# Kernel optimization log

Hardware: AMD Instinct MI355X
Metric: run time of the kernel (lower is better)

Reference implementation:

```python
import jax, jax.numpy as jnp
import numpy as np

K_EDE = 10.0   # self.k
T_EDE = 0.1    # self.t
BN_EPS = 1e-5
T_A = 576.0    # 3*3*64, hardcoded in my_bn1/my_bn2


def qfn(x, prec):
    # dorefa-style round quantizer with straight-through gradient
    n = float(2 ** prec - 1)
    return x + jax.lax.stop_gradient(jnp.round(x * n) / n - x)


@jax.custom_vjp
def binary_quantize(x):
    return jnp.sign(x)


def _bq_fwd(x):
    return jnp.sign(x), x


def _bq_bwd(x, g):
    # IR-Net EDE backward: k * t * (1 - tanh(x*t)^2)
    return (K_EDE * T_EDE * (1.0 - jnp.tanh(x * T_EDE) ** 2) * g,)


binary_quantize.defvjp(_bq_fwd, _bq_bwd)


def _clip_T(x):
    T = jnp.maximum(jnp.abs(x.min()), jnp.abs(x.max()))
    return jax.lax.stop_gradient(jnp.clip(T, 1e-10, 255.0))


def quantize_conv_act(x, prec):
    # my_quantize_conv: clamp to [-T, T], scale to [-1,1], qfn (no rescale by T)
    T = _clip_T(x)
    return qfn(jnp.clip(x, -T, T) / T, prec)


def quantize(x, prec):
    # my_quantize: same but rescaled back by T
    T = _clip_T(x)
    return qfn(jnp.clip(x, -T, T) / T, prec) * T


def ir_conv2d(a, w, stride):
    # IR-Net 1w8a IRConv2d: per-out-channel normalize, binarize (sign), power-of-2 scale
    co = w.shape[0]
    wf = w.reshape(co, -1)
    bw = (w - wf.mean(1)[:, None, None, None]) / jnp.std(wf, axis=1, ddof=1)[:, None, None, None]
    sw = jax.lax.stop_gradient(
        2.0 ** jnp.round(jnp.log2(jnp.abs(bw.reshape(co, -1)).mean(1)))
    )[:, None, None, None]
    bw = binary_quantize(bw) * sw
    return jax.lax.conv_general_dilated(
        a, bw, window_strides=(stride, stride), padding=[(1, 1), (1, 1)],
        dimension_numbers=('NCHW', 'OIHW', 'NCHW'))


def bn_as_quantized_affine(x, gamma, beta, mean, var):
    # my_bn1/my_bn2 (eval mode): BN folded into per-channel scale+bias.
    # The original builds a CxC diagonal 1x1 conv; since off-diagonal entries are 0,
    # both the quantization stats (max|.|) and the conv reduce exactly to this
    # per-channel affine, which is the faithful fused form.
    std = jnp.sqrt(var + BN_EPS)
    w = gamma / std
    b = beta - w * mean
    qw = quantize(w, 3)
    qb = quantize(b, 12)
    aq = qfn(x / T_A, 10) * T_A  # my_quantize_activation(input, 10, T_a)
    return aq * qw[None, :, None, None] + qb[None, :, None, None]


def _block(x, w1, w2, g1, b1, m1, v1, g2, b2, m2, v2):
    xq = quantize_conv_act(x, 3)
    out = ir_conv2d(xq, w1, 1)
    out = bn_as_quantized_affine(out, g1, b1, m1, v1) + xq  # identity shortcut
    out = jnp.clip(out, -1.0, 1.0)  # hardtanh
    x1 = quantize_conv_act(out, 3)
    out = ir_conv2d(x1, w2, 1)
    out = bn_as_quantized_affine(out, g2, b2, m2, v2) + x1
    return jnp.clip(out, -1.0, 1.0)


def setup_inputs() -> dict:
    key = jax.random.key(0)
    ks = jax.random.split(key, 11)
    B, C, H, W = 128, 64, 56, 56
    return {
        'x': jax.random.normal(ks[0], (B, C, H, W), jnp.float32),
        'w1': jax.random.normal(ks[1], (C, C, 3, 3), jnp.float32) * 0.1,
        'w2': jax.random.normal(ks[2], (C, C, 3, 3), jnp.float32) * 0.1,
        'g1': jax.random.uniform(ks[3], (C,), jnp.float32, 0.5, 1.5),
        'b1': jax.random.normal(ks[4], (C,), jnp.float32) * 0.1,
        'm1': jax.random.normal(ks[5], (C,), jnp.float32) * 0.1,
        'v1': jax.random.uniform(ks[6], (C,), jnp.float32, 0.5, 1.5),
        'g2': jax.random.uniform(ks[7], (C,), jnp.float32, 0.5, 1.5),
        'b2': jax.random.normal(ks[8], (C,), jnp.float32) * 0.1,
        'm2': jax.random.normal(ks[9], (C,), jnp.float32) * 0.1,
        'v2': jax.random.uniform(ks[10], (C,), jnp.float32, 0.5, 1.5),
    }


def reference(x, w1, w2, g1, b1, m1, v1, g2, b2, m2, v2):
    return _block(x, w1, w2, g1, b1, m1, v1, g2, b2, m2, v2)
```

## Files before the change

### kernel.cpp

```cpp
#include <hip/hip_runtime.h>
#include <stdint.h>

typedef int v4i   __attribute__((ext_vector_type(4)));
typedef int v16i  __attribute__((ext_vector_type(16)));

#define B_    128
#define C_    64
#define H_    56
#define W_    56
#define HW_   3136
#define NELEM (B_*C_*HW_)

#define OFF_K0   0
#define OFF_K1   ((size_t)NELEM)
#define OFF_WB   ((size_t)2*NELEM)
#define OFF_PAR  (OFF_WB + 2*4*9*64*16)
#define OFF_MAX  (OFF_PAR + 384*4)

__device__ __forceinline__ float pw_reduce64(float r) {
    r = __fadd_rn(r, __shfl_xor(r, 1, 64));
    r = __fadd_rn(r, __shfl_xor(r, 2, 64));
    r = __fadd_rn(r, __shfl_xor(r, 4, 64));
    r = __fadd_rn(r, __shfl_xor(r, 8, 64));
    r = __fadd_rn(r, __shfl_xor(r, 16, 64));
    r = __fadd_rn(r, __shfl_xor(r, 32, 64));
    return r;
}

__global__ void k_pre(const float* __restrict__ x, unsigned* __restrict__ maxbits,
                      const float* __restrict__ w1, const float* __restrict__ w2,
                      int8_t* __restrict__ wb, float* __restrict__ par,
                      const float* __restrict__ g1, const float* __restrict__ bb1,
                      const float* __restrict__ mm1, const float* __restrict__ vv1,
                      const float* __restrict__ g2, const float* __restrict__ bb2,
                      const float* __restrict__ mm2, const float* __restrict__ vv2) {
    __shared__ float smax[4];
    const int b = blockIdx.x;
    const int tid = threadIdx.x;
    if (b < 1024) {
        float m = 0.f;
        const int n4 = NELEM / 4;
        for (int i = b * 256 + tid; i < n4; i += 1024 * 256) {
            float4 v = ((const float4*)x)[i];
            m = fmaxf(m, fmaxf(fmaxf(fabsf(v.x), fabsf(v.y)), fmaxf(fabsf(v.z), fabsf(v.w))));
        }
        for (int off = 32; off; off >>= 1) m = fmaxf(m, __shfl_down(m, off, 64));
        if ((tid & 63) == 0) smax[tid >> 6] = m;
        __syncthreads();
        if (tid == 0) {
            float mm = fmaxf(fmaxf(smax[0], smax[1]), fmaxf(smax[2], smax[3]));
            atomicMax(maxbits, __float_as_uint(mm));
        }
    } else if (b < 1056) {
        const int idx = (b - 1024) * 4 + (tid >> 6);
        const int layer = idx >> 6, co = idx & 63;
        const int lane = tid & 63;
        const float* w = (layer ? w2 : w1) + (size_t)co * 576;
        const int base = (lane >> 3) * 72 + (lane & 7);

        float v[9];
#pragma unroll
        for (int i = 0; i < 9; i++) v[i] = w[base + 8 * i];

        float s = v[0];
#pragma unroll
        for (int i = 1; i < 9; i++) s = __fadd_rn(s, v[i]);
        const float mean = __fdiv_rn(pw_reduce64(s), 576.0f);

        float d0 = __fsub_rn(v[0], mean);
        float sq = __fmul_rn(d0, d0);
#pragma unroll
        for (int i = 1; i < 9; i++) {
            float d = __fsub_rn(v[i], mean);
            sq = __fadd_rn(sq, __fmul_rn(d, d));
        }
        const float sig = __fsqrt_rn(__fdiv_rn(pw_reduce64(sq), 575.0f));

        float sa = fabsf(__fdiv_rn(__fsub_rn(v[0], mean), sig));
#pragma unroll
        for (int i = 1; i < 9; i++)
            sa = __fadd_rn(sa, fabsf(__fdiv_rn(__fsub_rn(v[i], mean), sig)));
        const float ma = __fdiv_rn(pw_reduce64(sa), 576.0f);
        const float p  = rintf(log2f(ma));
        if (lane == 0) par[256 + layer * 64 + co] = __fdiv_rn(exp2f(p), 7.0f);

#pragma unroll
        for (int i = 0; i < 9; i++) {
            int ig = base + 8 * i;
            float d = __fsub_rn(v[i], mean);
            int8_t sg = (d > 0.0f) ? (int8_t)1 : ((d < 0.0f) ? (int8_t)-1 : (int8_t)0);
            int ci = ig / 9, tp = ig % 9;
            wb[((((size_t)layer * 4 + (ci >> 4)) * 9 + tp) * 64 + co) * 16 + (ci & 15)] = sg;
        }
    } else {
        if (tid < 128) {
            const int layer = tid >> 6;
            const int c = tid & 63;
            const float* g  = layer ? g2  : g1;
            const float* be = layer ? bb2 : bb1;
            const float* mu = layer ? mm2 : mm1;
            const float* va = layer ? vv2 : vv1;
            const float stdv = __fsqrt_rn(__fadd_rn(va[c], 1e-5f));
            const float w = __fdiv_rn(g[c], stdv);
            const float bb = __fsub_rn(be[c], __fmul_rn(w, mu[c]));
            float aw = fabsf(w), ab = fabsf(bb);
            for (int off = 32; off; off >>= 1) {
                aw = fmaxf(aw, __shfl_xor(aw, off, 64));
                ab = fmaxf(ab, __shfl_xor(ab, off, 64));
            }
            const float Tw = fminf(fmaxf(aw, 1e-10f), 255.0f);
            const float Tb = fminf(fmaxf(ab, 1e-10f), 255.0f);
            {
                float vq = __fdiv_rn(fminf(fmaxf(w, -Tw), Tw), Tw);
                float r  = rintf(__fmul_rn(vq, 7.0f));
                float qf = __fadd_rn(vq, __fsub_rn(__fdiv_rn(r, 7.0f), vq));
                par[layer * 64 + c] = __fmul_rn(qf, Tw);
            }
            {
                float vq = __fdiv_rn(fminf(fmaxf(bb, -Tb), Tb), Tb);
                float r  = rintf(__fmul_rn(vq, 4095.0f));
                float qf = __fadd_rn(vq, __fsub_rn(__fdiv_rn(r, 4095.0f), vq));
                par[128 + layer * 64 + c] = __fmul_rn(qf, Tb);
            }
        }
    }
}

__global__ void k_quant(const float* __restrict__ x, const unsigned* __restrict__ maxbits,
                        int8_t* __restrict__ k8) {
    __shared__ unsigned tile[56 * 17];
    const int n = blockIdx.x / H_;
    const int y = blockIdx.x % H_;
    const float T = fminf(fmaxf(__uint_as_float(*maxbits), 1e-10f), 255.0f);
    const double dinv = 1.0 / (double)T;
    const int t = threadIdx.x;
    if (t < 224) {
        const int cb = t / 14, xb = t % 14;
        const float* src = x + ((size_t)(n * 64 + 4 * cb)) * HW_ + y * 56 + 4 * xb;
        int kq[4][4];
#pragma unroll
        for (int i = 0; i < 4; i++) {
            float4 v = *(const float4*)(src + (size_t)i * HW_);
            const float e[4] = {v.x, v.y, v.z, v.w};
#pragma unroll
            for (int j = 0; j < 4; j++) {
                const float tc = fminf(fmaxf(e[j], -T), T);
                const float u  = (float)((double)tc * dinv);
                kq[i][j] = (int)rintf(__fmul_rn(u, 7.0f));
            }
        }
#pragma unroll
        for (int j = 0; j < 4; j++) {
            const unsigned d = (kq[0][j] & 255) | ((kq[1][j] & 255) << 8) |
                               ((kq[2][j] & 255) << 16) | ((unsigned)(kq[3][j] & 255) << 24);
            tile[(4 * xb + j) * 17 + cb] = d;
        }
    }
    __syncthreads();
    unsigned* dst = (unsigned*)(k8 + ((size_t)(n * 56 + y)) * 56 * 64);
    for (int u = t; u < 896; u += 256)
        dst[u] = tile[(u >> 4) * 17 + (u & 15)];
}

template <int LAYER>
__global__ __launch_bounds__(896, 7) void k_conv(const int8_t* __restrict__ kin,
                                                 const int8_t* __restrict__ wb,
                                                 const float* __restrict__ par,
                                                 int8_t* __restrict__ kout,
                                                 float* __restrict__ fout) {
    __shared__ __align__(16) int8_t halo[4 * 10 * 58 * 16];
    __shared__ __align__(16) int8_t wsm[4 * 9 * 64 * 16];
    const int n  = blockIdx.x / 7;
    const int y0 = (blockIdx.x % 7) * 8;
    const int tid = threadIdx.x;

    for (int u = tid; u < 2320; u += 896) {
        const int q = u & 3, v = u >> 2;
        const int r = v / 58, xp = v % 58;
        const int y = y0 - 1 + r, xg = xp - 1;
        int4 val = {0, 0, 0, 0};
        if (y >= 0 && y < 56 && xg >= 0 && xg < 56)
            val = *(const int4*)(kin + (((size_t)(n * 56 + y)) * 56 + xg) * 64 + q * 16);
        *(int4*)(halo + (((q * 10 + r) * 58 + xp) << 4)) = val;
    }
    const int8_t* wsrc = wb + (size_t)(LAYER - 1) * (4 * 9 * 64 * 16);
    for (int u = tid; u < 2304; u += 896)
        *(int4*)(wsm + u * 16) = *(const int4*)(wsrc + u * 16);
    __syncthreads();

    const int wv = tid >> 6, lane = tid & 63;
    const int mbase = wv * 32;
    const int ml = lane & 31;
    const int khalf = lane >> 5;
    const int m = mbase + ml;
    const int rm = m / 56, cm = m % 56;

    v16i acc0, acc1;
#pragma unroll
    for (int i = 0; i < 16; i++) { acc0[i] = 0; acc1[i] = 0; }

#pragma unroll
    for (int s = 0; s < 9; s++) {
        const int ky = s / 3, kx = s % 3;
#pragma unroll
        for (int kb = 0; kb < 2; kb++) {
            const int q = khalf + 2 * kb;
            v4i a  = *(const v4i*)(halo + ((((q * 10 + rm + ky) * 58) + cm + kx) << 4));
            v4i b0 = *(const v4i*)(wsm  + (((q * 9 + s) * 64 + ml) << 4));
            v4i b1 = *(const v4i*)(wsm  + (((q * 9 + s) * 64 + 32 + ml) << 4));
            acc0 = __builtin_amdgcn_mfma_i32_32x32x32_i8(a, b0, acc0, 0, 0, 0);
            acc1 = __builtin_amdgcn_mfma_i32_32x32x32_i8(a, b1, acc1, 0, 0, 0);
        }
    }

    const float* qw = par + (LAYER - 1) * 64;
    const float* qb = par + 128 + (LAYER - 1) * 64;
    const float* sc = par + 256 + (LAYER - 1) * 64;
#pragma unroll
    for (int t = 0; t < 2; t++) {
        const int co = ml + t * 32;
        const float qwf = qw[co], qbf = qb[co], scf = sc[co];
        const int qc = co >> 4, cl = co & 15;
        const int clw = cl & ~3, cb8 = (cl & 3) * 8;
#pragma unroll
        for (int g = 0; g < 4; g++) {
            const int mb = mbase + 8 * g + 4 * khalf;
            const int rloc = mb / 56;
            const int cl0  = mb % 56;
            const int pixbase = (qc * 10 + rloc + 1) * 58 + cl0 + 1;
            float vals[4];
#pragma unroll
            for (int i = 0; i < 4; i++) {
                const int   S  = t ? acc1[4 * g + i] : acc0[4 * g + i];
                const float Sf = (float)S;
                const float convf = __fmul_rn(Sf, scf);
                const float xb = (float)((double)convf * (1.0 / 576.0));
                const float rr = rintf(__fmul_rn(xb, 1023.0f));
                const float q1 = (float)((double)rr * (1.0 / 1023.0));
                const float y1 = __fadd_rn(xb, __fsub_rn(q1, xb));
                const float aq = __fmul_rn(y1, 576.0f);
                const unsigned wd = *(const unsigned*)(halo + ((pixbase + i) << 4) + clw);
                const int   kc = (int)(int8_t)(wd >> cb8);
                const float xqv = (float)((double)kc * (1.0 / 7.0));
                float val = __fadd_rn(__fadd_rn(__fmul_rn(aq, qwf), qbf), xqv);
                val = fminf(fmaxf(val, -1.0f), 1.0f);
                if (LAYER == 1) {
                    const int k2 = (int)rintf(__fmul_rn(val, 7.0f));
                    kout[(((size_t)(n * 56 + y0 + rloc)) * 56 + cl0 + i) * 64 + co] = (int8_t)k2;
                } else {
                    vals[i] = val;
                }
            }
            if (LAYER == 2) {
                float4 o = make_float4(vals[0], vals[1], vals[2], vals[3]);
                *(float4*)(fout + ((size_t)(n * 64 + co)) * HW_ + (y0 + rloc) * 56 + cl0) = o;
            }
        }
    }
}

extern "C" void kernel_launch(void* const* d_in, const int* in_sizes, int n_in,
                              void* d_out, int out_size, void* d_ws, size_t ws_size,
                              hipStream_t stream) {
    const float* x  = (const float*)d_in[0];
    const float* w1 = (const float*)d_in[1];
    const float* w2 = (const float*)d_in[2];
    const float* g1 = (const float*)d_in[3];
    const float* b1 = (const float*)d_in[4];
    const float* m1 = (const float*)d_in[5];
    const float* v1 = (const float*)d_in[6];
    const float* g2 = (const float*)d_in[7];
    const float* b2 = (const float*)d_in[8];
    const float* m2 = (const float*)d_in[9];
    const float* v2 = (const float*)d_in[10];

    char* ws = (char*)d_ws;
    int8_t*  k0  = (int8_t*)(ws + OFF_K0);
    int8_t*  k1  = (int8_t*)(ws + OFF_K1);
    int8_t*  wbp = (int8_t*)(ws + OFF_WB);
    float*   par = (float*)(ws + OFF_PAR);
    unsigned* mx = (unsigned*)(ws + OFF_MAX);

    hipMemsetAsync(mx, 0, 4, stream);
    k_pre<<<1057, 256, 0, stream>>>(x, mx, w1, w2, wbp, par,
                                    g1, b1, m1, v1, g2, b2, m2, v2);
    k_quant<<<B_ * H_, 256, 0, stream>>>(x, mx, k0);
    k_conv<1><<<B_ * 7, 896, 0, stream>>>(k0, wbp, par, k1, nullptr);
    k_conv<2><<<B_ * 7, 896, 0, stream>>>(k1, wbp, par, nullptr, (float*)d_out);
}
```

Before: 302.3 us.

## Make conv blocks persistent over row tiles with double-buffered halo prefetch

Each conv block now handles a strip of 3 or 4 consecutive 8-row tiles for one image instead of a single tile. It loads the weights into shared memory once and prefetches the next tile's halo into registers while the current tile runs its MFMA and epilogue, then stores it into a second shared-memory buffer. This amortises the weight load and hides global-load latency, but the grid drops from 896 to 256 blocks on a many-CU GPU. The extra halo buffer and prefetch registers may also reduce occupancy, and the 4-versus-3 tile split leaves some blocks with less work than others.

```diff
diff --git a/kernel.cpp b/kernel.cpp
--- a/kernel.cpp
+++ b/kernel.cpp
@@ -163,30 +163,18 @@
 }
 
 template <int LAYER>
-__global__ __launch_bounds__(896, 7) void k_conv(const int8_t* __restrict__ kin,
+__global__ __launch_bounds__(896, 4) void k_conv(const int8_t* __restrict__ kin,
                                                  const int8_t* __restrict__ wb,
                                                  const float* __restrict__ par,
                                                  int8_t* __restrict__ kout,
                                                  float* __restrict__ fout) {
-    __shared__ __align__(16) int8_t halo[4 * 10 * 58 * 16];
+    __shared__ __align__(16) int8_t halo[2][4 * 10 * 58 * 16];
     __shared__ __align__(16) int8_t wsm[4 * 9 * 64 * 16];
-    const int n  = blockIdx.x / 7;
-    const int y0 = (blockIdx.x % 7) * 8;
+    const int n     = blockIdx.x >> 1;
+    const int strip = blockIdx.x & 1;
+    const int nt    = strip ? 3 : 4;
+    const int ybase = strip ? 32 : 0;
     const int tid = threadIdx.x;
-
-    for (int u = tid; u < 2320; u += 896) {
-        const int q = u & 3, v = u >> 2;
-        const int r = v / 58, xp = v % 58;
-        const int y = y0 - 1 + r, xg = xp - 1;
-        int4 val = {0, 0, 0, 0};
-        if (y >= 0 && y < 56 && xg >= 0 && xg < 56)
-            val = *(const int4*)(kin + (((size_t)(n * 56 + y)) * 56 + xg) * 64 + q * 16);
-        *(int4*)(halo + (((q * 10 + r) * 58 + xp) << 4)) = val;
-    }
-    const int8_t* wsrc = wb + (size_t)(LAYER - 1) * (4 * 9 * 64 * 16);
-    for (int u = tid; u < 2304; u += 896)
-        *(int4*)(wsm + u * 16) = *(const int4*)(wsrc + u * 16);
-    __syncthreads();
 
     const int wv = tid >> 6, lane = tid & 63;
     const int mbase = wv * 32;
@@ -195,68 +183,120 @@
     const int m = mbase + ml;
     const int rm = m / 56, cm = m % 56;
 
-    v16i acc0, acc1;
-#pragma unroll
-    for (int i = 0; i < 16; i++) { acc0[i] = 0; acc1[i] = 0; }
-
-#pragma unroll
-    for (int s = 0; s < 9; s++) {
-        const int ky = s / 3, kx = s % 3;
-#pragma unroll
-        for (int kb = 0; kb < 2; kb++) {
-            const int q = khalf + 2 * kb;
-            v4i a  = *(const v4i*)(halo + ((((q * 10 + rm + ky) * 58) + cm + kx) << 4));
-            v4i b0 = *(const v4i*)(wsm  + (((q * 9 + s) * 64 + ml) << 4));
-            v4i b1 = *(const v4i*)(wsm  + (((q * 9 + s) * 64 + 32 + ml) << 4));
-            acc0 = __builtin_amdgcn_mfma_i32_32x32x32_i8(a, b0, acc0, 0, 0, 0);
-            acc1 = __builtin_amdgcn_mfma_i32_32x32x32_i8(a, b1, acc1, 0, 0, 0);
-        }
+    int4 pre[3];
+#define HALO_LOAD(Y0) do {                                                     \
+    _Pragma("unroll")                                                          \
+    for (int it = 0; it < 3; ++it) {                                           \
+        const int u = tid + it * 896;                                          \
+        int4 val = {0, 0, 0, 0};                                               \
+        if (u < 2320) {                                                        \
+            const int q = u & 3, vv = u >> 2;                                  \
+            const int r = vv / 58, xp = vv % 58;                               \
+            const int y = (Y0) - 1 + r, xg = xp - 1;                           \
+            if (y >= 0 && y < 56 && xg >= 0 && xg < 56)                        \
+                val = *(const int4*)(kin + (((size_t)(n * 56 + y)) * 56 + xg) * 64 + q * 16); \
+        }                                                                      \
+        pre[it] = val;                                                         \
+    }                                                                          \
+} while (0)
+#define HALO_WRITE(BUF) do {                                                   \
+    _Pragma("unroll")                                                          \
+    for (int it = 0; it < 3; ++it) {                                           \
+        const int u = tid + it * 896;                                          \
+        if (u < 2320) {                                                        \
+            const int q = u & 3, vv = u >> 2;                                  \
+            const int r = vv / 58, xp = vv % 58;                               \
+            *(int4*)((BUF) + (((q * 10 + r) * 58 + xp) << 4)) = pre[it];       \
+        }                                                                      \
+    }                                                                          \
+} while (0)
+
+    const int8_t* wsrc = wb + (size_t)(LAYER - 1) * (4 * 9 * 64 * 16);
+#pragma unroll
+    for (int it = 0; it < 3; ++it) {
+        const int u = tid + it * 896;
+        if (u < 2304) *(int4*)(wsm + u * 16) = *(const int4*)(wsrc + u * 16);
     }
+    HALO_LOAD(ybase);
+    HALO_WRITE(halo[0]);
+    __syncthreads();
 
     const float* qw = par + (LAYER - 1) * 64;
     const float* qb = par + 128 + (LAYER - 1) * 64;
     const float* sc = par + 256 + (LAYER - 1) * 64;
-#pragma unroll
-    for (int t = 0; t < 2; t++) {
-        const int co = ml + t * 32;
-        const float qwf = qw[co], qbf = qb[co], scf = sc[co];
-        const int qc = co >> 4, cl = co & 15;
-        const int clw = cl & ~3, cb8 = (cl & 3) * 8;
-#pragma unroll
-        for (int g = 0; g < 4; g++) {
-            const int mb = mbase + 8 * g + 4 * khalf;
-            const int rloc = mb / 56;
-            const int cl0  = mb % 56;
-            const int pixbase = (qc * 10 + rloc + 1) * 58 + cl0 + 1;
-            float vals[4];
-#pragma unroll
-            for (int i = 0; i < 4; i++) {
-                const int   S  = t ? acc1[4 * g + i] : acc0[4 * g + i];
-                const float Sf = (float)S;
-                const float convf = __fmul_rn(Sf, scf);
-                const float xb = (float)((double)convf * (1.0 / 576.0));
-                const float rr = rintf(__fmul_rn(xb, 1023.0f));
-                const float q1 = (float)((double)rr * (1.0 / 1023.0));
-                const float y1 = __fadd_rn(xb, __fsub_rn(q1, xb));
-                const float aq = __fmul_rn(y1, 576.0f);
-                const unsigned wd = *(const unsigned*)(halo + ((pixbase + i) << 4) + clw);
-                const int   kc = (int)(int8_t)(wd >> cb8);
-                const float xqv = (float)((double)kc * (1.0 / 7.0));
-                float val = __fadd_rn(__fadd_rn(__fmul_rn(aq, qwf), qbf), xqv);
-                val = fminf(fmaxf(val, -1.0f), 1.0f);
-                if (LAYER == 1) {
-                    const int k2 = (int)rintf(__fmul_rn(val, 7.0f));
-                    kout[(((size_t)(n * 56 + y0 + rloc)) * 56 + cl0 + i) * 64 + co] = (int8_t)k2;
-                } else {
-                    vals[i] = val;
+
+    for (int tt = 0; tt < nt; ++tt) {
+        const int y0 = ybase + tt * 8;
+        if (tt + 1 < nt) HALO_LOAD(y0 + 8);
+        const int8_t* hb = halo[tt & 1];
+
+        v16i acc0, acc1;
+#pragma unroll
+        for (int i = 0; i < 16; i++) { acc0[i] = 0; acc1[i] = 0; }
+
+#pragma unroll
+        for (int s = 0; s < 9; s++) {
+            const int ky = s / 3, kx = s % 3;
+#pragma unroll
+            for (int kb = 0; kb < 2; kb++) {
+                const int q = khalf + 2 * kb;
+                v4i a  = *(const v4i*)(hb  + ((((q * 10 + rm + ky) * 58) + cm + kx) << 4));
+                v4i b0 = *(const v4i*)(wsm + (((q * 9 + s) * 64 + ml) << 4));
+                v4i b1 = *(const v4i*)(wsm + (((q * 9 + s) * 64 + 32 + ml) << 4));
+                acc0 = __builtin_amdgcn_mfma_i32_32x32x32_i8(a, b0, acc0, 0, 0, 0);
+                acc1 = __builtin_amdgcn_mfma_i32_32x32x32_i8(a, b1, acc1, 0, 0, 0);
+            }
+        }
+
+#pragma unroll
+        for (int th = 0; th < 2; th++) {
+            const int co = ml + th * 32;
+            const float qwf = qw[co], qbf = qb[co], scf = sc[co];
+            const int qc = co >> 4, cl = co & 15;
+            const int clw = cl & ~3, cb8 = (cl & 3) * 8;
+#pragma unroll
+            for (int g = 0; g < 4; g++) {
+                const int mb = mbase + 8 * g + 4 * khalf;
+                const int rloc = mb / 56;
+                const int cl0  = mb % 56;
+                const int pixbase = (qc * 10 + rloc + 1) * 58 + cl0 + 1;
+                float vals[4];
+#pragma unroll
+                for (int i = 0; i < 4; i++) {
+                    const int   S  = th ? acc1[4 * g + i] : acc0[4 * g + i];
+                    const float Sf = (float)S;
+                    const float convf = __fmul_rn(Sf, scf);
+                    const float xb = (float)((double)convf * (1.0 / 576.0));
+                    const float rr = rintf(__fmul_rn(xb, 1023.0f));
+                    const float q1 = (float)((double)rr * (1.0 / 1023.0));
+                    const float y1 = __fadd_rn(xb, __fsub_rn(q1, xb));
+                    const float aq = __fmul_rn(y1, 576.0f);
+                    const unsigned wd = *(const unsigned*)(hb + ((pixbase + i) << 4) + clw);
+                    const int   kc = (int)(int8_t)(wd >> cb8);
+                    const float xqv = (float)((double)kc * (1.0 / 7.0));
+                    float val = __fadd_rn(__fadd_rn(__fmul_rn(aq, qwf), qbf), xqv);
+                    val = fminf(fmaxf(val, -1.0f), 1.0f);
+                    if (LAYER == 1) {
+                        const int k2 = (int)rintf(__fmul_rn(val, 7.0f));
+                        kout[(((size_t)(n * 56 + y0 + rloc)) * 56 + cl0 + i) * 64 + co] = (int8_t)k2;
+                    } else {
+                        vals[i] = val;
+                    }
                 }
-            }
-            if (LAYER == 2) {
-                float4 o = make_float4(vals[0], vals[1], vals[2], vals[3]);
-                *(float4*)(fout + ((size_t)(n * 64 + co)) * HW_ + (y0 + rloc) * 56 + cl0) = o;
-            }
+                if (LAYER == 2) {
+                    float4 o = make_float4(vals[0], vals[1], vals[2], vals[3]);
+                    *(float4*)(fout + ((size_t)(n * 64 + co)) * HW_ + (y0 + rloc) * 56 + cl0) = o;
+                }
+            }
+        }
+
+        if (tt + 1 < nt) {
+            HALO_WRITE(halo[(tt + 1) & 1]);
+            __syncthreads();
         }
     }
+#undef HALO_LOAD
+#undef HALO_WRITE
 }
 
 extern "C" void kernel_launch(void* const* d_in, const int* in_sizes, int n_in,
@@ -285,6 +325,6 @@
     k_pre<<<1057, 256, 0, stream>>>(x, mx, w1, w2, wbp, par,
                                     g1, b1, m1, v1, g2, b2, m2, v2);
     k_quant<<<B_ * H_, 256, 0, stream>>>(x, mx, k0);
-    k_conv<1><<<B_ * 7, 896, 0, stream>>>(k0, wbp, par, k1, nullptr);
-    k_conv<2><<<B_ * 7, 896, 0, stream>>>(k1, wbp, par, nullptr, (float*)d_out);
-}
+    k_conv<1><<<B_ * 2, 896, 0, stream>>>(k0, wbp, par, k1, nullptr);
+    k_conv<2><<<B_ * 2, 896, 0, stream>>>(k1, wbp, par, nullptr, (float*)d_out);
+}
```

After: 311.7 us. +3.1%, slower.
